# Optimization experiments

Hardware: AMD Instinct MI355X
Metric: run time of the kernel (lower is better)

The kernel has to match this reference:

```python
import jax, jax.numpy as jnp
import numpy as np
from jax import lax

B, T, INPUT, HIDDEN, OUT = 8192, 512, 10, 64, 1


def setup_inputs() -> dict:
    key = jax.random.key(0)
    k1, k2, k3, k4, k5 = jax.random.split(key, 5)
    padded_batch = jax.random.normal(k1, (B, T, INPUT), dtype=jnp.float32)
    lengths = jax.random.randint(k2, (B,), 1, T + 1, dtype=jnp.int64)
    # per-timestep distinct RNN weights, init scale 0.01 as in the torch module
    W_xh = jax.random.normal(k3, (T, INPUT, HIDDEN), dtype=jnp.float32) * 0.01
    W_hh = jax.random.normal(k4, (T, HIDDEN, HIDDEN), dtype=jnp.float32) * 0.01
    W_lin = jax.random.normal(k5, (HIDDEN, OUT), dtype=jnp.float32) * (1.0 / np.sqrt(HIDDEN))
    b_lin = jnp.zeros((OUT,), dtype=jnp.float32)
    return {"padded_batch": padded_batch, "lengths": lengths,
            "W_xh": W_xh, "W_hh": W_hh, "W_lin": W_lin, "b_lin": b_lin}


def reference(padded_batch, lengths, W_xh, W_hh, W_lin, b_lin):
    # padded_batch: [B, T, INPUT]; per-step weights W_xh: [T, INPUT, H], W_hh: [T, H, H]
    Bn = padded_batch.shape[0]
    x_tbd = jnp.swapaxes(padded_batch, 0, 1)  # [T, B, INPUT]
    t_idx = jnp.arange(T)

    def step(h, inputs):
        x_t, wxh, whh, t = inputs
        new_h = jnp.tanh(x_t @ wxh + h @ whh)          # [B, H]
        keep = (t < lengths)[:, None]                   # freeze samples past their length
        h = jnp.where(keep, new_h, h)
        return h, None

    h0 = jnp.zeros((Bn, HIDDEN), dtype=padded_batch.dtype)
    last_hidden, _ = lax.scan(step, h0, (x_tbd, W_xh, W_hh, t_idx))
    return last_hidden @ W_lin + b_lin  # [B, OUT]
```

## Files before the change

kernel.cpp:

```cpp
#include <hip/hip_runtime.h>
#include <stdint.h>

#define T_STEPS 512
#define HID     64
#define INP     10
#define MB      16
#define KS      88
#define HS      72
#define XS      40
#define WT_ELEMS (HID*KS)
#define WT_BYTES (WT_ELEMS*2)
#define WS_SLOTS (WT_BYTES/16)

typedef float  f32x4  __attribute__((ext_vector_type(4)));
typedef short  s16x8  __attribute__((ext_vector_type(8)));
typedef __bf16 bf16x8 __attribute__((ext_vector_type(8)));

__device__ __forceinline__ short f2bf(float f) {
    unsigned u = __builtin_bit_cast(unsigned, f);
    u = (u + 0x7FFFu + ((u >> 16) & 1u)) >> 16;
    return (short)u;
}
__device__ __forceinline__ float bf2f(short s) {
    unsigned u = ((unsigned)(unsigned short)s) << 16;
    return __builtin_bit_cast(float, u);
}

__global__ __launch_bounds__(256) void prep_w(const float* __restrict__ Wxh,
                                              const float* __restrict__ Whh,
                                              short* __restrict__ Wc) {
    __shared__ float s_hh[64 * 64];
    __shared__ float s_xh[INP * 64];
    const int t = blockIdx.x, tid = threadIdx.x;
    for (int i = tid; i < 64 * 64; i += 256) s_hh[i] = Whh[t * 4096 + i];
    for (int i = tid; i < INP * 64; i += 256) s_xh[i] = Wxh[t * (INP * 64) + i];
    __syncthreads();
    short* dst = Wc + (size_t)t * WT_ELEMS;
    for (int i = tid; i < WT_ELEMS; i += 256) {
        const int n = i / KS, k = i % KS;
        float v = 0.f;
        if (k < 64)      v = s_hh[k * 64 + n];
        else if (k < 74) v = s_xh[(k - 64) * 64 + n];
        dst[i] = f2bf(v);
    }
}

__global__ __launch_bounds__(256, 2) void rnn_main(const float* __restrict__ X,
                                                   const int* __restrict__ L,
                                                   const short* __restrict__ Wc,
                                                   const float* __restrict__ Wlin,
                                                   const float* __restrict__ blin,
                                                   float* __restrict__ out) {
    __shared__ __attribute__((aligned(16))) short Wb[2][WT_ELEMS + 16];
    __shared__ __attribute__((aligned(16))) short hb[2][MB * HS];
    __shared__ __attribute__((aligned(16))) short xb[2][MB * XS];
    __shared__ int len_s[MB];

    const int tid  = threadIdx.x;
    const int lane = tid & 63;
    const int wv   = tid >> 6;
    const int q    = lane >> 4;
    const int l    = lane & 15;
    const long long bbase = (long long)blockIdx.x * MB;

    for (int i = tid; i < MB * HS; i += 256) hb[0][i] = 0;
    for (int i = tid; i < MB * XS; i += 256) { xb[0][i] = 0; xb[1][i] = 0; }
    if (tid < 16) { Wb[0][WT_ELEMS + tid] = 0; Wb[1][WT_ELEMS + tid] = 0; }
    if (tid < MB) len_s[tid] = L[bbase + tid];
    __syncthreads();

    {
        const char* src = (const char*)(Wc);
        char* dst = (char*)&Wb[0][0];
#pragma unroll
        for (int i = 0; i < 3; ++i) {
            const int slot = tid + i * 256;
            if (slot < WS_SLOTS)
                __builtin_amdgcn_global_load_lds(
                    (const __attribute__((address_space(1))) unsigned int*)(src + slot * 16),
                    (__attribute__((address_space(3))) unsigned int*)(dst + slot * 16),
                    16, 0, 0);
        }
    }
    const int xs = tid / INP, xi = tid % INP;
    float xreg = 0.f;
    if (tid < MB * INP) {
        xb[0][xs * XS + xi] = f2bf(X[(bbase + xs) * (T_STEPS * INP) + 0 * INP + xi]);
        xreg = X[(bbase + xs) * (T_STEPS * INP) + 1 * INP + xi];
    }
    __syncthreads();

    float hc[4] = {0.f, 0.f, 0.f, 0.f};
    int len4[4];
#pragma unroll
    for (int r = 0; r < 4; ++r) len4[r] = len_s[q * 4 + r];
    const int colw = wv * 16 + l;

    for (int t = 0; t < T_STEPS; ++t) {
        const int cur = t & 1, nxt = cur ^ 1;

        if (t + 1 < T_STEPS) {
            const char* src = (const char*)(Wc) + (size_t)(t + 1) * WT_BYTES;
            char* dst = (char*)&Wb[nxt][0];
#pragma unroll
            for (int i = 0; i < 3; ++i) {
                const int slot = tid + i * 256;
                if (slot < WS_SLOTS)
                    __builtin_amdgcn_global_load_lds(
                        (const __attribute__((address_space(1))) unsigned int*)(src + slot * 16),
                        (__attribute__((address_space(3))) unsigned int*)(dst + slot * 16),
                        16, 0, 0);
            }
        }

        if (tid < MB * INP) {
            xb[nxt][xs * XS + xi] = f2bf(xreg);
            if (t + 2 < T_STEPS)
                xreg = X[(bbase + xs) * (T_STEPS * INP) + (long long)(t + 2) * INP + xi];
        }

        const s16x8 a0 = *(const s16x8*)&hb[cur][l * HS + q * 8];
        const s16x8 a1 = *(const s16x8*)&hb[cur][l * HS + 32 + q * 8];
        const s16x8 a2 = *(const s16x8*)&xb[cur][l * XS + q * 8];
        const s16x8 b0 = *(const s16x8*)&Wb[cur][colw * KS + q * 8];
        const s16x8 b1 = *(const s16x8*)&Wb[cur][colw * KS + 32 + q * 8];
        const s16x8 b2 = *(const s16x8*)&Wb[cur][colw * KS + 64 + q * 8];

        f32x4 z = {0.f, 0.f, 0.f, 0.f};
        f32x4 acc0 = __builtin_amdgcn_mfma_f32_16x16x32_bf16(
                  __builtin_bit_cast(bf16x8, a0), __builtin_bit_cast(bf16x8, b0), z, 0, 0, 0);
        f32x4 acc1 = __builtin_amdgcn_mfma_f32_16x16x32_bf16(
                  __builtin_bit_cast(bf16x8, a1), __builtin_bit_cast(bf16x8, b1), z, 0, 0, 0);
        f32x4 acc2 = __builtin_amdgcn_mfma_f32_16x16x32_bf16(
                  __builtin_bit_cast(bf16x8, a2), __builtin_bit_cast(bf16x8, b2), z, 0, 0, 0);

#pragma unroll
        for (int r = 0; r < 4; ++r) {
            const float a  = acc0[r] + acc1[r] + acc2[r];
            const float e  = __expf(2.f * a);
            const float th = 1.f - 2.f * __builtin_amdgcn_rcpf(e + 1.f);
            hc[r] = (t < len4[r]) ? th : hc[r];
            hb[nxt][(q * 4 + r) * HS + colw] = f2bf(hc[r]);
        }
        __syncthreads();
    }

    const float wl = Wlin[lane];
    const float bl = blin[0];
#pragma unroll
    for (int it = 0; it < 4; ++it) {
        const int s = wv + it * 4;
        float v = bf2f(hb[0][s * HS + lane]) * wl;
#pragma unroll
        for (int off = 32; off > 0; off >>= 1) v += __shfl_down(v, off);
        if (lane == 0) out[bbase + s] = v + bl;
    }
}

extern "C" void kernel_launch(void* const* d_in, const int* in_sizes, int n_in,
                              void* d_out, int out_size, void* d_ws, size_t ws_size,
                              hipStream_t stream) {
    const float* X    = (const float*)d_in[0];
    const int*   L    = (const int*)d_in[1];
    const float* Wxh  = (const float*)d_in[2];
    const float* Whh  = (const float*)d_in[3];
    const float* Wlin = (const float*)d_in[4];
    const float* blin = (const float*)d_in[5];
    float*       out  = (float*)d_out;
    short*       Wc   = (short*)d_ws;

    prep_w<<<T_STEPS, 256, 0, stream>>>(Wxh, Whh, Wc);
    rnn_main<<<8192 / MB, 256, 0, stream>>>(X, L, Wc, Wlin, blin, out);
}
```

Before: 590.5 us.

## Batch input loads into 8-step chunks and add polynomial tanh fast path

Input rows are now fetched once every 8 timesteps with vectorized nontemporal 16-byte loads into a double-buffered shared chunk, replacing a scalar global load and shared store on every step. The tanh switches to an odd polynomial whenever every preactivation in the wave is at most 0.55 in magnitude, avoiding exp and reciprocal on the serial critical path. The weight-prep kernel pads its shared transpose buffers to avoid bank conflicts. In exchange the kernel uses more shared memory and adds a wave-wide vote and branch on every step.

```diff
diff --git a/kernel.cpp b/kernel.cpp
--- a/kernel.cpp
+++ b/kernel.cpp
@@ -5,14 +5,17 @@
 #define HID     64
 #define INP     10
 #define MB      16
+#define CH      8
 #define KS      88
 #define HS      72
 #define XS      40
 #define WT_ELEMS (HID*KS)
 #define WT_BYTES (WT_ELEMS*2)
 #define WS_SLOTS (WT_BYTES/16)
+#define XC_ELEMS (CH*MB*XS)
 
 typedef float  f32x4  __attribute__((ext_vector_type(4)));
+typedef float  f32x4v __attribute__((ext_vector_type(4)));
 typedef short  s16x8  __attribute__((ext_vector_type(8)));
 typedef __bf16 bf16x8 __attribute__((ext_vector_type(8)));
 
@@ -29,18 +32,18 @@
 __global__ __launch_bounds__(256) void prep_w(const float* __restrict__ Wxh,
                                               const float* __restrict__ Whh,
                                               short* __restrict__ Wc) {
-    __shared__ float s_hh[64 * 64];
-    __shared__ float s_xh[INP * 64];
+    __shared__ float s_hh[64 * 65];
+    __shared__ float s_xh[INP * 65];
     const int t = blockIdx.x, tid = threadIdx.x;
-    for (int i = tid; i < 64 * 64; i += 256) s_hh[i] = Whh[t * 4096 + i];
-    for (int i = tid; i < INP * 64; i += 256) s_xh[i] = Wxh[t * (INP * 64) + i];
+    for (int i = tid; i < 64 * 64; i += 256) s_hh[(i >> 6) * 65 + (i & 63)] = Whh[t * 4096 + i];
+    for (int i = tid; i < INP * 64; i += 256) s_xh[(i >> 6) * 65 + (i & 63)] = Wxh[t * (INP * 64) + i];
     __syncthreads();
     short* dst = Wc + (size_t)t * WT_ELEMS;
     for (int i = tid; i < WT_ELEMS; i += 256) {
         const int n = i / KS, k = i % KS;
         float v = 0.f;
-        if (k < 64)      v = s_hh[k * 64 + n];
-        else if (k < 74) v = s_xh[(k - 64) * 64 + n];
+        if (k < 64)      v = s_hh[k * 65 + n];
+        else if (k < 74) v = s_xh[(k - 64) * 65 + n];
         dst[i] = f2bf(v);
     }
 }
@@ -53,7 +56,7 @@
                                                    float* __restrict__ out) {
     __shared__ __attribute__((aligned(16))) short Wb[2][WT_ELEMS + 16];
     __shared__ __attribute__((aligned(16))) short hb[2][MB * HS];
-    __shared__ __attribute__((aligned(16))) short xb[2][MB * XS];
+    __shared__ __attribute__((aligned(16))) short xc[2][XC_ELEMS];
     __shared__ int len_s[MB];
 
     const int tid  = threadIdx.x;
@@ -62,9 +65,10 @@
     const int q    = lane >> 4;
     const int l    = lane & 15;
     const long long bbase = (long long)blockIdx.x * MB;
+    const float* Xblk = X + bbase * (T_STEPS * INP);
 
     for (int i = tid; i < MB * HS; i += 256) hb[0][i] = 0;
-    for (int i = tid; i < MB * XS; i += 256) { xb[0][i] = 0; xb[1][i] = 0; }
+    for (int i = tid; i < 2 * XC_ELEMS; i += 256) ((short*)xc)[i] = 0;
     if (tid < 16) { Wb[0][WT_ELEMS + tid] = 0; Wb[1][WT_ELEMS + tid] = 0; }
     if (tid < MB) len_s[tid] = L[bbase + tid];
     __syncthreads();
@@ -82,11 +86,19 @@
                     16, 0, 0);
         }
     }
-    const int xs = tid / INP, xi = tid % INP;
-    float xreg = 0.f;
-    if (tid < MB * INP) {
-        xb[0][xs * XS + xi] = f2bf(X[(bbase + xs) * (T_STEPS * INP) + 0 * INP + xi]);
-        xreg = X[(bbase + xs) * (T_STEPS * INP) + 1 * INP + xi];
+#pragma unroll
+    for (int it = 0; it < 2; ++it) {
+        const int slot = tid + it * 256;
+        if (slot < MB * 20) {
+            const int s = slot / 20, d = slot % 20;
+            const f32x4v v = __builtin_nontemporal_load(
+                (const f32x4v*)(Xblk + s * (T_STEPS * INP)) + d);
+#pragma unroll
+            for (int j = 0; j < 4; ++j) {
+                const int e = d * 4 + j;
+                xc[0][((e / 10) * MB + s) * XS + (e % 10)] = f2bf(v[j]);
+            }
+        }
     }
     __syncthreads();
 
@@ -98,6 +110,7 @@
 
     for (int t = 0; t < T_STEPS; ++t) {
         const int cur = t & 1, nxt = cur ^ 1;
+        const int cb  = (t >> 3) & 1;
 
         if (t + 1 < T_STEPS) {
             const char* src = (const char*)(Wc) + (size_t)(t + 1) * WT_BYTES;
@@ -113,15 +126,28 @@
             }
         }
 
-        if (tid < MB * INP) {
-            xb[nxt][xs * XS + xi] = f2bf(xreg);
-            if (t + 2 < T_STEPS)
-                xreg = X[(bbase + xs) * (T_STEPS * INP) + (long long)(t + 2) * INP + xi];
+        if ((t & 7) == 0 && t <= (T_STEPS - 2 * CH)) {
+            const int t0 = t + CH;
+            short* dstc = &xc[cb ^ 1][0];
+#pragma unroll
+            for (int it = 0; it < 2; ++it) {
+                const int slot = tid + it * 256;
+                if (slot < MB * 20) {
+                    const int s = slot / 20, d = slot % 20;
+                    const f32x4v v = __builtin_nontemporal_load(
+                        (const f32x4v*)(Xblk + s * (T_STEPS * INP) + t0 * INP) + d);
+#pragma unroll
+                    for (int j = 0; j < 4; ++j) {
+                        const int e = d * 4 + j;
+                        dstc[((e / 10) * MB + s) * XS + (e % 10)] = f2bf(v[j]);
+                    }
+                }
+            }
         }
 
         const s16x8 a0 = *(const s16x8*)&hb[cur][l * HS + q * 8];
         const s16x8 a1 = *(const s16x8*)&hb[cur][l * HS + 32 + q * 8];
-        const s16x8 a2 = *(const s16x8*)&xb[cur][l * XS + q * 8];
+        const s16x8 a2 = *(const s16x8*)&xc[cb][((t & 7) * MB + l) * XS + q * 8];
         const s16x8 b0 = *(const s16x8*)&Wb[cur][colw * KS + q * 8];
         const s16x8 b1 = *(const s16x8*)&Wb[cur][colw * KS + 32 + q * 8];
         const s16x8 b2 = *(const s16x8*)&Wb[cur][colw * KS + 64 + q * 8];
@@ -134,12 +160,30 @@
         f32x4 acc2 = __builtin_amdgcn_mfma_f32_16x16x32_bf16(
                   __builtin_bit_cast(bf16x8, a2), __builtin_bit_cast(bf16x8, b2), z, 0, 0, 0);
 
+        float av[4], th[4];
+#pragma unroll
+        for (int r = 0; r < 4; ++r) av[r] = acc0[r] + acc1[r] + acc2[r];
+        const float mx = fmaxf(fmaxf(fabsf(av[0]), fabsf(av[1])),
+                               fmaxf(fabsf(av[2]), fabsf(av[3])));
+        if (__any(mx > 0.55f)) {
+#pragma unroll
+            for (int r = 0; r < 4; ++r) {
+                const float e = __expf(2.f * av[r]);
+                th[r] = 1.f - 2.f * __builtin_amdgcn_rcpf(e + 1.f);
+            }
+        } else {
+#pragma unroll
+            for (int r = 0; r < 4; ++r) {
+                const float a = av[r], s = a * a;
+                float p = fmaf(s, 0.02186948f, -0.05396825f);
+                p = fmaf(s, p, 0.13333334f);
+                p = fmaf(s, p, -0.33333334f);
+                th[r] = fmaf(a * s, p, a);
+            }
+        }
 #pragma unroll
         for (int r = 0; r < 4; ++r) {
-            const float a  = acc0[r] + acc1[r] + acc2[r];
-            const float e  = __expf(2.f * a);
-            const float th = 1.f - 2.f * __builtin_amdgcn_rcpf(e + 1.f);
-            hc[r] = (t < len4[r]) ? th : hc[r];
+            hc[r] = (t < len4[r]) ? th[r] : hc[r];
             hb[nxt][(q * 4 + r) * HS + colw] = f2bf(hc[r]);
         }
         __syncthreads();
```

Result: slower. 608.6 us (+3.1%).
